# Kernel tuning notes

Hardware: AMD Instinct MI355X
Metric: run time of the kernel (lower is better)

## Reference

```python
import jax, jax.numpy as jnp
import numpy as np

EMBED_DIM = 768
NUM_HEADS = 12
HEAD_DIM = EMBED_DIM // NUM_HEADS
EPS = 1e-5  # nn.LayerNorm default


def setup_inputs() -> dict:
    key = jax.random.key(0)
    ks = jax.random.split(key, 7)
    D = EMBED_DIM
    s1 = 1.0 / np.sqrt(D)
    x = jax.random.normal(ks[0], (2, 2048, D), dtype=jnp.float32)
    # LayerNorm params
    gamma = jnp.ones((D,), jnp.float32)
    beta = jnp.zeros((D,), jnp.float32)
    # QKV projection (linear1): weight [3D, D], bias [3D]
    w1 = jax.random.uniform(ks[1], (3 * D, D), jnp.float32, -s1, s1)
    b1 = jax.random.uniform(ks[2], (3 * D,), jnp.float32, -s1, s1)
    # Output projection (linear2[0]): weight [D, D], bias [D]
    w2 = jax.random.uniform(ks[3], (D, D), jnp.float32, -s1, s1)
    b2 = jax.random.uniform(ks[4], (D,), jnp.float32, -s1, s1)
    return {"x": x, "gamma": gamma, "beta": beta, "w1": w1, "b1": b1, "w2": w2, "b2": b2}


def _layernorm(x, gamma, beta):
    mu = jnp.mean(x, axis=-1, keepdims=True)
    var = jnp.mean(jnp.square(x - mu), axis=-1, keepdims=True)
    return (x - mu) * jax.lax.rsqrt(var + EPS) * gamma + beta


def reference(x, gamma, beta, w1, b1, w2, b2) -> jnp.ndarray:
    B, L, D = x.shape
    H, Dh = NUM_HEADS, HEAD_DIM
    residual = x
    h = _layernorm(x, gamma, beta)
    qkv = h @ w1.T + b1  # [B, L, 3D]
    q, k, v = jnp.split(qkv, 3, axis=-1)
    # 'b n (h d) -> b h n d'
    q = q.reshape(B, L, H, Dh).transpose(0, 2, 1, 3)
    k = k.reshape(B, L, H, Dh).transpose(0, 2, 1, 3)
    v = v.reshape(B, L, H, Dh).transpose(0, 2, 1, 3)
    scores = jnp.einsum("bhqd,bhkd->bhqk", q, k) / jnp.sqrt(jnp.float32(Dh))
    attn = jax.nn.softmax(scores, axis=-1)  # dropout is identity in eval mode
    out = jnp.einsum("bhqk,bhkd->bhqd", attn, v)  # [B, H, L, Dh]
    out = out.transpose(0, 2, 1, 3).reshape(B, L, D)
    out = out @ w2.T + b2  # dropout identity in eval
    return residual + out
```

## Files before the change

kernel.cpp:

```cpp
#include <hip/hip_runtime.h>


#define DEV __device__ __forceinline__

typedef __attribute__((ext_vector_type(4))) float f32x4;
typedef __attribute__((ext_vector_type(8))) short s16x8;
typedef __attribute__((ext_vector_type(2))) int i32x2;

constexpr int Bb   = 2;
constexpr int Ll   = 2048;
constexpr int Dd   = 768;
constexpr int Hh   = 12;
constexpr int Dh   = 64;
constexpr int Mrows = Bb * Ll;
constexpr int N1   = 3 * Dd;

DEV unsigned short f2bf(float f) {
  union { float f; unsigned u; } v; v.f = f;
  unsigned r = v.u + 0x7fffu + ((v.u >> 16) & 1u);
  return (unsigned short)(r >> 16);
}

DEV void gload_lds16(const void* g, void* l) {
  __builtin_amdgcn_global_load_lds((const __attribute__((address_space(1))) unsigned int*)g,
                                   (__attribute__((address_space(3))) unsigned int*)l,
                                   16, 0, 0);
}

DEV f32x4 mfma16(s16x8 a, s16x8 b, f32x4 c) {
  return __builtin_amdgcn_mfma_f32_16x16x32_bf16(a, b, c, 0, 0, 0);
}

DEV float fexp2(float x) { float r; asm("v_exp_f32 %0, %1" : "=v"(r) : "v"(x)); return r; }
DEV float frcp(float x)  { float r; asm("v_rcp_f32 %0, %1" : "=v"(r) : "v"(x)); return r; }

DEV float redmax64(float x) {
  x = fmaxf(x, __shfl_xor(x, 16, 64));
  float a = x, b = x;
  asm volatile("v_permlane32_swap_b32 %0, %1" : "+v"(a), "+v"(b));
  return fmaxf(a, b);
}
DEV float redsum64(float x) {
  x += __shfl_xor(x, 16, 64);
  float a = x, b = x;
  asm volatile("v_permlane32_swap_b32 %0, %1" : "+v"(a), "+v"(b));
  return a + b;
}

DEV void ln_body(int row, int t, const float* __restrict__ x,
                 const float* __restrict__ gamma, const float* __restrict__ beta,
                 short* __restrict__ hbuf, float* red) {
  const float* xr = x + (size_t)row * Dd;
  float v0 = xr[t], v1 = xr[t + 256], v2 = xr[t + 512];
  float s = v0 + v1 + v2;
  float q = v0 * v0 + v1 * v1 + v2 * v2;
#pragma unroll
  for (int off = 32; off; off >>= 1) {
    s += __shfl_xor(s, off, 64);
    q += __shfl_xor(q, off, 64);
  }
  const int w = t >> 6, lane = t & 63;
  if (lane == 0) { red[w] = s; red[4 + w] = q; }
  __syncthreads();
  s = red[0] + red[1] + red[2] + red[3];
  q = red[4] + red[5] + red[6] + red[7];
  const float mean = s * (1.f / Dd);
  const float var  = q * (1.f / Dd) - mean * mean;
  const float rstd = rsqrtf(var + 1e-5f);
  short* hr = hbuf + (size_t)row * Dd;
  hr[t]       = (short)f2bf((v0 - mean) * rstd * gamma[t]       + beta[t]);
  hr[t + 256] = (short)f2bf((v1 - mean) * rstd * gamma[t + 256] + beta[t + 256]);
  hr[t + 512] = (short)f2bf((v2 - mean) * rstd * gamma[t + 512] + beta[t + 512]);
}

constexpr int W1E = N1 * Dd;
constexpr int W2E = Dd * Dd;

__global__ __launch_bounds__(256) void ln_kernel(const float* __restrict__ x,
                                                 const float* __restrict__ gamma,
                                                 const float* __restrict__ beta,
                                                 short* __restrict__ hbuf) {
  __shared__ float red[8];
  ln_body(blockIdx.x, threadIdx.x, x, gamma, beta, hbuf, red);
}

__global__ __launch_bounds__(256) void cvt_kernel(const float* __restrict__ w1,
                                                  const float* __restrict__ w2,
                                                  short* __restrict__ w1b,
                                                  short* __restrict__ w2b) {
  int i = blockIdx.x * 256 + threadIdx.x;
  const int stride = gridDim.x * 256;
  for (; i < W1E + W2E; i += stride) {
    if (i < W1E) w1b[i] = (short)f2bf(w1[i]);
    else         w2b[i - W1E] = (short)f2bf(w2[i - W1E]);
  }
}

__global__ __launch_bounds__(256) void prep_kernel(const float* __restrict__ x,
                                                   const float* __restrict__ gamma,
                                                   const float* __restrict__ beta,
                                                   short* __restrict__ hbuf,
                                                   const float* __restrict__ w1,
                                                   const float* __restrict__ w2,
                                                   short* __restrict__ w1b,
                                                   short* __restrict__ w2b) {
  __shared__ float red[8];
  if (blockIdx.x < (unsigned)Mrows) {
    ln_body(blockIdx.x, threadIdx.x, x, gamma, beta, hbuf, red);
  } else {
    int i = (blockIdx.x - Mrows) * 256 + threadIdx.x;
    for (; i < W1E + W2E; i += 1024 * 256) {
      if (i < W1E) w1b[i] = (short)f2bf(w1[i]);
      else         w2b[i - W1E] = (short)f2bf(w2[i - W1E]);
    }
  }
}

DEV unsigned xcd_swz(unsigned f, unsigned nwg) {
  if ((nwg & 7u) != 0u) return f;
  return (f & 7u) * (nwg >> 3) + (f >> 3);
}

template <int EPI, int WSRC>
__global__ __launch_bounds__(256) void gemm_bt(const short* __restrict__ A,
                                               const void* __restrict__ Wp,
                                               const float* __restrict__ bias,
                                               const float* __restrict__ resid,
                                               void* __restrict__ outp,
                                               int N, int K) {
  __shared__ __align__(16) short As[2][WSRC == 0 ? 128 * 32 : 128 * 64];
  __shared__ __align__(16) short Ws[2][WSRC == 0 ? 128 * 32 : 128 * 64];
  const int tid  = threadIdx.x;
  const int lane = tid & 63, wid = tid >> 6;
  const int wr = wid >> 1, wc = wid & 1;
  const int g = lane >> 4, li = lane & 15;
  const unsigned o = xcd_swz(blockIdx.y * gridDim.x + blockIdx.x,
                             gridDim.x * gridDim.y);
  const int brow = (int)(o / gridDim.x) * 128, bcol = (int)(o % gridDim.x) * 128;

  f32x4 acc[4][4];
#pragma unroll
  for (int m = 0; m < 4; ++m)
#pragma unroll
    for (int n = 0; n < 4; ++n)
#pragma unroll
      for (int r = 0; r < 4; ++r) acc[m][n][r] = 0.f;

  if constexpr (WSRC == 0) {
    const short* W = (const short*)Wp;
    const int nt = K >> 5;
    auto stage = [&](int t, int buf) {
      const int ko = t << 5;
#pragma unroll
      for (int i = 0; i < 2; ++i) {
        const int idx = i * 256 + tid;
        const int r = idx >> 2, c = idx & 3;
        const int cs = c ^ ((r >> 1) & 3);
        gload_lds16(A + (size_t)(brow + r) * K + ko + cs * 8,
                    (char*)&As[buf][0] + idx * 16);
        gload_lds16(W + (size_t)(bcol + r) * K + ko + cs * 8,
                    (char*)&Ws[buf][0] + idx * 16);
      }
    };
    stage(0, 0);
    stage(1, 1);
    for (int it = 0; it < nt; ++it) {
      const int cur = it & 1;
      if (it + 1 < nt) asm volatile("s_waitcnt vmcnt(4)" ::: "memory");
      else             asm volatile("s_waitcnt vmcnt(0)" ::: "memory");
      __builtin_amdgcn_s_barrier();
      __builtin_amdgcn_sched_barrier(0);
      {
        s16x8 af[4], bf[4];
        const int rsw = ((li >> 1) & 3);
#pragma unroll
        for (int m = 0; m < 4; ++m) {
          const int row = wr * 64 + m * 16 + li;
          af[m] = *(const s16x8*)((char*)&As[cur][0] + row * 64 + ((g ^ rsw) << 4));
        }
#pragma unroll
        for (int n = 0; n < 4; ++n) {
          const int row = wc * 64 + n * 16 + li;
          bf[n] = *(const s16x8*)((char*)&Ws[cur][0] + row * 64 + ((g ^ rsw) << 4));
        }
#pragma unroll
        for (int m = 0; m < 4; ++m)
#pragma unroll
          for (int n = 0; n < 4; ++n)
            acc[m][n] = mfma16(af[m], bf[n], acc[m][n]);
      }
      __builtin_amdgcn_s_barrier();
      if (it + 2 < nt) stage(it + 2, cur);
    }
  } else {
    const float* W = (const float*)Wp;
    for (int kt = 0; kt < K; kt += 64) {
#pragma unroll
      for (int i = 0; i < 4; ++i) {
        const int idx = i * 256 + tid;
        const int r = idx >> 3, c = idx & 7;
        const int cs = c ^ (r & 7);
        gload_lds16(A + (size_t)(brow + r) * K + kt + cs * 8,
                    (char*)&As[0][0] + idx * 16);
      }
#pragma unroll
      for (int i = 0; i < 4; ++i) {
        const int idx = i * 256 + tid;
        const int r = idx >> 3, c = idx & 7;
        const float* wp = W + (size_t)(bcol + r) * K + kt + c * 8;
        const f32x4 lo = *(const f32x4*)wp;
        const f32x4 hi = *(const f32x4*)(wp + 4);
        s16x8 oo;
#pragma unroll
        for (int j = 0; j < 4; ++j) {
          oo[j]     = (short)f2bf(lo[j]);
          oo[4 + j] = (short)f2bf(hi[j]);
        }
        *(s16x8*)((char*)&Ws[0][0] + (size_t)(r * 8 + (c ^ (r & 7))) * 16) = oo;
      }
      __syncthreads();
#pragma unroll
      for (int kk = 0; kk < 2; ++kk) {
        s16x8 af[4], bf[4];
#pragma unroll
        for (int m = 0; m < 4; ++m) {
          const int row = wr * 64 + m * 16 + li;
          af[m] = *(const s16x8*)&As[0][row * 64 + (((kk * 4 + g) ^ (li & 7)) & 7) * 8];
        }
#pragma unroll
        for (int n = 0; n < 4; ++n) {
          const int row = wc * 64 + n * 16 + li;
          bf[n] = *(const s16x8*)&Ws[0][row * 64 + (((kk * 4 + g) ^ (li & 7)) & 7) * 8];
        }
#pragma unroll
        for (int m = 0; m < 4; ++m)
#pragma unroll
          for (int n = 0; n < 4; ++n)
            acc[m][n] = mfma16(af[m], bf[n], acc[m][n]);
      }
      __syncthreads();
    }
  }

#pragma unroll
  for (int m = 0; m < 4; ++m) {
#pragma unroll
    for (int n = 0; n < 4; ++n) {
      const int col = bcol + wc * 64 + n * 16 + li;
      const float bv = bias[col];
#pragma unroll
      for (int r = 0; r < 4; ++r) {
        const int row = brow + wr * 64 + m * 16 + g * 4 + r;
        const float v = acc[m][n][r] + bv;
        if (EPI == 0) {
          ((short*)outp)[(size_t)row * N + col] = (short)f2bf(v);
        } else {
          const size_t o2 = (size_t)row * N + col;
          ((float*)outp)[o2] = v + resid[o2];
        }
      }
    }
  }
}

#define TRRD(dst, addr, OFF)                                                   \
  asm volatile("ds_read_b64_tr_b16 %0, %1 offset:" #OFF                        \
               : "=v"(dst) : "v"(addr))

__global__ __launch_bounds__(256) void attn_kernel(const short* __restrict__ qkv,
                                                   short* __restrict__ obuf) {
  __shared__ __align__(16) short Ks[2][64 * 64];
  __shared__ __align__(16) short Vt[2][64 * 64];
  __shared__ __align__(16) short Ps[4][16 * 64];
  const int tid  = threadIdx.x;
  const int lane = tid & 63, w = tid >> 6;
  const int g = lane >> 4, li = lane & 15;
  const unsigned o = xcd_swz(blockIdx.y * 32u + blockIdx.x, gridDim.x * gridDim.y);
  const int bh = (int)(o >> 5);
  const int b = bh / Hh, h = bh % Hh;
  const size_t rowbase = (size_t)b * Ll * N1;
  const int q0 = (int)(o & 31u) * 64 + w * 16;
  constexpr float kScale = 0.125f * 1.44269504f;
  constexpr float kThrRaw = 8.f / kScale;
  constexpr int KVSTRIDE = 64 * N1;

  s16x8 qf[2];
#pragma unroll
  for (int ks = 0; ks < 2; ++ks)
    qf[ks] = *(const s16x8*)(qkv + rowbase + (size_t)(q0 + li) * N1 +
                             h * Dh + ks * 32 + g * 8);

  f32x4 oa[4];
  float m_ = -1e30f, l_ = 0.f;
#pragma unroll
  for (int dn = 0; dn < 4; ++dn)
#pragma unroll
    for (int r = 0; r < 4; ++r) oa[dn][r] = 0.f;

  constexpr int NT = Ll / 64;

  const int ia = tid, ib = 256 + tid;
  const int ra = ia >> 3, ca = ia & 7, rb = ib >> 3, cb = ib & 7;
  const short* kpa = qkv + rowbase + Dd + h * Dh + (size_t)ra * N1 + (ca ^ (ra & 7)) * 8;
  const short* kpb = qkv + rowbase + Dd + h * Dh + (size_t)rb * N1 + (cb ^ (rb & 7)) * 8;
  const int Ta = ia >> 3, Tb = ib >> 3;
  const short* vpa = qkv + rowbase + 2 * Dd + h * Dh +
                     (size_t)((Ta & 15) * 4 + (ca >> 1)) * N1 + (Ta >> 4) * 16 + (ia & 1) * 8;
  const short* vpb = qkv + rowbase + 2 * Dd + h * Dh +
                     (size_t)((Tb & 15) * 4 + (cb >> 1)) * N1 + (Tb >> 4) * 16 + (ib & 1) * 8;
  char* KsB = (char*)&Ks[0][0];
  char* VtB = (char*)&Vt[0][0];
  const int dsta = ia * 16, dstb = ib * 16;

  int koff[4][2];
#pragma unroll
  for (int n = 0; n < 4; ++n) {
    koff[n][0] = ((n * 16 + li) * 64 + ((g ^ (li & 7)) & 7) * 8) * 2;
    koff[n][1] = ((n * 16 + li) * 64 + (((4 + g) ^ (li & 7)) & 7) * 8) * 2;
  }
  int pwoff[4], proff[2];
#pragma unroll
  for (int n = 0; n < 4; ++n)
    pwoff[n] = li * 128 + (((2 * n + (g >> 1)) ^ (li & 7)) << 4) + 8 * (g & 1);
#pragma unroll
  for (int kk = 0; kk < 2; ++kk)
    proff[kk] = li * 128 + (((4 * kk + g) ^ (li & 7)) << 4);
  char* Pw = (char*)&Ps[w][0];
  const unsigned vlane = (unsigned)((lane >> 4) * 256 + (lane & 15) * 2);
  const unsigned vbase0 = (unsigned)(unsigned long long)(&Vt[0][0]) + vlane;

  auto stageK = [&](int buf) {
    const int bo = buf << 13;
    gload_lds16(kpa, KsB + bo + dsta);
    gload_lds16(kpb, KsB + bo + dstb);
    kpa += KVSTRIDE; kpb += KVSTRIDE;
  };
  auto stageV = [&](int buf) {
    const int bo = buf << 13;
    gload_lds16(vpa, VtB + bo + dsta);
    gload_lds16(vpb, VtB + bo + dstb);
    vpa += KVSTRIDE; vpb += KVSTRIDE;
  };

  stageK(0); stageV(0); stageK(1); stageV(1);
  asm volatile("s_waitcnt vmcnt(4)" ::: "memory");
  __builtin_amdgcn_s_barrier();
  __builtin_amdgcn_sched_barrier(0);

  f32x4 zA[4], zB[4];
#pragma unroll
  for (int n = 0; n < 4; ++n) {
    s16x8 kf0 = *(const s16x8*)(KsB + koff[n][0]);
    s16x8 kf1 = *(const s16x8*)(KsB + koff[n][1]);
    f32x4 z;
#pragma unroll
    for (int r = 0; r < 4; ++r) z[r] = 0.f;
    z = mfma16(kf0, qf[0], z);
    z = mfma16(kf1, qf[1], z);
    zA[n] = z;
  }

  auto body = [&](int kt, int cur, f32x4 (&zC)[4], f32x4 (&zN)[4]) {
    const int curo = cur << 13;
    const int nxto = (cur ^ 1) << 13;
    if (kt + 1 < NT) asm volatile("s_waitcnt vmcnt(2)" ::: "memory");
    else             asm volatile("s_waitcnt vmcnt(0)" ::: "memory");
    __builtin_amdgcn_s_barrier();
    __builtin_amdgcn_sched_barrier(0);

    if (kt + 2 < NT) stageK(cur);

    if (kt + 1 < NT) {
      __builtin_amdgcn_s_setprio(1);
#pragma unroll
      for (int n = 0; n < 4; ++n) {
        s16x8 kf0 = *(const s16x8*)(KsB + nxto + koff[n][0]);
        s16x8 kf1 = *(const s16x8*)(KsB + nxto + koff[n][1]);
        f32x4 z;
#pragma unroll
        for (int r = 0; r < 4; ++r) z[r] = 0.f;
        z = mfma16(kf0, qf[0], z);
        z = mfma16(kf1, qf[1], z);
        zN[n] = z;
      }
      __builtin_amdgcn_s_setprio(0);
    }

    const float t0 = fmaxf(fmaxf(zC[0][0], zC[0][1]), zC[0][2]);
    const float t1 = fmaxf(fmaxf(zC[0][3], zC[1][0]), zC[1][1]);
    const float t2 = fmaxf(fmaxf(zC[1][2], zC[1][3]), zC[2][0]);
    const float t3 = fmaxf(fmaxf(zC[2][1], zC[2][2]), zC[2][3]);
    const float t4 = fmaxf(fmaxf(zC[3][0], zC[3][1]), zC[3][2]);
    const float mloc = fmaxf(fmaxf(fmaxf(fmaxf(t0, t1), t2), fmaxf(t3, t4)), zC[3][3]);
    if (!__all(mloc - m_ <= kThrRaw)) {
      const float mxr = redmax64(mloc);
      const float mnew = fmaxf(m_, mxr);
      const float sc = fexp2((m_ - mnew) * kScale);
      float scq[4];
#pragma unroll
      for (int r = 0; r < 4; ++r)
        scq[r] = __shfl(sc, (lane & 48) + ((lane & 48) >> 2) + r, 64);
#pragma unroll
      for (int dn = 0; dn < 4; ++dn)
#pragma unroll
        for (int r = 0; r < 4; ++r) oa[dn][r] *= scq[r];
      l_ *= sc;
      m_ = mnew;
    }
    const float msc = m_ * kScale;
#pragma unroll
    for (int n = 0; n < 4; ++n)
#pragma unroll
      for (int r = 0; r < 4; ++r) {
        const float p = fexp2(fmaf(zC[n][r], kScale, -msc));
        zC[n][r] = p;
        l_ += p;
      }

#pragma unroll
    for (int n = 0; n < 4; ++n) {
      unsigned u0, u1;
      asm("v_cvt_pk_bf16_f32 %0, %1, %2" : "=v"(u0) : "v"(zC[n][0]), "v"(zC[n][1]));
      asm("v_cvt_pk_bf16_f32 %0, %1, %2" : "=v"(u1) : "v"(zC[n][2]), "v"(zC[n][3]));
      i32x2 pv; pv[0] = (int)u0; pv[1] = (int)u1;
      *(i32x2*)(Pw + pwoff[n]) = pv;
    }

    s16x8 pf[2];
#pragma unroll
    for (int kk = 0; kk < 2; ++kk)
      pf[kk] = *(const s16x8*)(Pw + proff[kk]);

    union VU { long l[2]; s16x8 v; };
    VU vu[4][2];
    {
      const unsigned vaddr = vbase0 + (unsigned)curo;
      TRRD(vu[0][0].l[0], vaddr, 0);    TRRD(vu[0][0].l[1], vaddr, 128);
      TRRD(vu[0][1].l[0], vaddr, 1024); TRRD(vu[0][1].l[1], vaddr, 1152);
      TRRD(vu[1][0].l[0], vaddr, 2048); TRRD(vu[1][0].l[1], vaddr, 2176);
      TRRD(vu[1][1].l[0], vaddr, 3072); TRRD(vu[1][1].l[1], vaddr, 3200);
      TRRD(vu[2][0].l[0], vaddr, 4096); TRRD(vu[2][0].l[1], vaddr, 4224);
      TRRD(vu[2][1].l[0], vaddr, 5120); TRRD(vu[2][1].l[1], vaddr, 5248);
      TRRD(vu[3][0].l[0], vaddr, 6144); TRRD(vu[3][0].l[1], vaddr, 6272);
      TRRD(vu[3][1].l[0], vaddr, 7168); TRRD(vu[3][1].l[1], vaddr, 7296);
    }
    asm volatile("s_waitcnt lgkmcnt(0)" ::: "memory");
    __builtin_amdgcn_sched_barrier(0);

    __builtin_amdgcn_s_setprio(1);
#pragma unroll
    for (int dn = 0; dn < 4; ++dn) {
      oa[dn] = mfma16(pf[0], vu[dn][0].v, oa[dn]);
      oa[dn] = mfma16(pf[1], vu[dn][1].v, oa[dn]);
    }
    __builtin_amdgcn_s_setprio(0);

    __builtin_amdgcn_s_barrier();
    if (kt + 2 < NT) stageV(cur);
  };

  for (int g2 = 0; g2 < NT / 2; ++g2) {
    body(2 * g2,     0, zA, zB);
    body(2 * g2 + 1, 1, zB, zA);
  }

  l_ = redsum64(l_);
  {
#pragma unroll
    for (int r = 0; r < 4; ++r) {
      const float lq = __shfl(l_, (lane & 48) + ((lane & 48) >> 2) + r, 64);
      const float inv = frcp(lq);
      const int row = b * Ll + q0 + g * 4 + r;
#pragma unroll
      for (int dn = 0; dn < 4; ++dn)
        obuf[(size_t)row * Dd + h * Dh + dn * 16 + li] =
            (short)f2bf(oa[dn][r] * inv);
    }
  }
}

extern "C" void kernel_launch(void* const* d_in, const int* in_sizes, int n_in,
                              void* d_out, int out_size, void* d_ws, size_t ws_size,
                              hipStream_t stream) {
  const float* x     = (const float*)d_in[0];
  const float* gamma = (const float*)d_in[1];
  const float* beta  = (const float*)d_in[2];
  const float* w1    = (const float*)d_in[3];
  const float* b1    = (const float*)d_in[4];
  const float* w2    = (const float*)d_in[5];
  const float* b2    = (const float*)d_in[6];
  float* out = (float*)d_out;
  char* ws = (char*)d_ws;

  if (ws_size >= 29884416) {
    short* qkvb = (short*)(ws);
    short* hb   = (short*)(ws + 18874368);
    short* w1b  = (short*)(ws + 25165824);
    short* w2b  = (short*)(ws + 28704768);
    prep_kernel<<<dim3(Mrows + 1024), dim3(256), 0, stream>>>(
        x, gamma, beta, hb, w1, w2, w1b, w2b);
    gemm_bt<0, 0><<<dim3(N1 / 128, Mrows / 128), dim3(256), 0, stream>>>(
        hb, w1b, b1, nullptr, (void*)qkvb, N1, Dd);
    attn_kernel<<<dim3(Ll / 64, Bb * Hh), dim3(256), 0, stream>>>(qkvb, hb);
    gemm_bt<1, 0><<<dim3(Dd / 128, Mrows / 128), dim3(256), 0, stream>>>(
        hb, w2b, b2, x, (void*)out, Dd, Dd);
  } else if (ws_size >= 17301504) {
    short* qkvb = (short*)(ws);
    short* hb   = (short*)(ws + 9437184);
    short* w1b  = (short*)(ws + 12582912);
    short* w2b  = (short*)(ws + 16121856);
    cvt_kernel<<<dim3(1024), dim3(256), 0, stream>>>(w1, w2, w1b, w2b);
    for (int b = 0; b < Bb; ++b) {
      const size_t ro = (size_t)b * Ll * Dd;
      ln_kernel<<<dim3(Ll), dim3(256), 0, stream>>>(x + ro, gamma, beta, hb);
      gemm_bt<0, 0><<<dim3(N1 / 128, Ll / 128), dim3(256), 0, stream>>>(
          hb, w1b, b1, nullptr, (void*)qkvb, N1, Dd);
      attn_kernel<<<dim3(Ll / 64, Hh), dim3(256), 0, stream>>>(qkvb, hb);
      gemm_bt<1, 0><<<dim3(Dd / 128, Ll / 128), dim3(256), 0, stream>>>(
          hb, w2b, b2, x + ro, (void*)(out + ro), Dd, Dd);
    }
  } else {
    short* qkvb = (short*)(ws);
    short* hb   = (short*)(ws + 9437184);
    for (int b = 0; b < Bb; ++b) {
      const size_t ro = (size_t)b * Ll * Dd;
      ln_kernel<<<dim3(Ll), dim3(256), 0, stream>>>(x + ro, gamma, beta, hb);
      gemm_bt<0, 1><<<dim3(N1 / 128, Ll / 128), dim3(256), 0, stream>>>(
          hb, w1, b1, nullptr, (void*)qkvb, N1, Dd);
      attn_kernel<<<dim3(Ll / 64, Hh), dim3(256), 0, stream>>>(qkvb, hb);
      gemm_bt<1, 1><<<dim3(Dd / 128, Ll / 128), dim3(256), 0, stream>>>(
          hb, w2, b2, x + ro, (void*)(out + ro), Dd, Dd);
    }
  }
}
```

Baseline: 101.6 us.

## Split attention KV range across two wave groups and vectorize weight conversion

The attention kernel now uses 512 threads per block. Two groups of four waves each process half of the key/value sequence for the same 64 query rows, with separate double-buffered K/V tiles in shared memory. A final flash-decoding style merge combines the partial max, sum and output through LDS. Separately, the fp32-to-bf16 weight conversion now loads float4 and uses packed bf16 convert instructions instead of scalar per-element stores. The aim is more parallelism and latency hiding per query tile and a cheaper prep stage, at the cost of doubled LDS use, which may lower occupancy, plus extra merge work.

```diff
diff --git a/kernel.cpp b/kernel.cpp
--- a/kernel.cpp
+++ b/kernel.cpp
@@ -75,6 +75,20 @@
 
 constexpr int W1E = N1 * Dd;
 constexpr int W2E = Dd * Dd;
+constexpr int WV4 = (W1E + W2E) / 4;
+
+DEV void cvt_v4(int i, const float* __restrict__ w1, const float* __restrict__ w2,
+                short* __restrict__ w1b, short* __restrict__ w2b) {
+  const int e = i * 4;
+  const float* src = (e < W1E) ? (w1 + e) : (w2 + (e - W1E));
+  short* dst       = (e < W1E) ? (w1b + e) : (w2b + (e - W1E));
+  const f32x4 v = *(const f32x4*)src;
+  unsigned u01, u23;
+  asm("v_cvt_pk_bf16_f32 %0, %1, %2" : "=v"(u01) : "v"(v[0]), "v"(v[1]));
+  asm("v_cvt_pk_bf16_f32 %0, %1, %2" : "=v"(u23) : "v"(v[2]), "v"(v[3]));
+  i32x2 o; o[0] = (int)u01; o[1] = (int)u23;
+  *(i32x2*)dst = o;
+}
 
 __global__ __launch_bounds__(256) void ln_kernel(const float* __restrict__ x,
                                                  const float* __restrict__ gamma,
@@ -90,10 +104,7 @@
                                                   short* __restrict__ w2b) {
   int i = blockIdx.x * 256 + threadIdx.x;
   const int stride = gridDim.x * 256;
-  for (; i < W1E + W2E; i += stride) {
-    if (i < W1E) w1b[i] = (short)f2bf(w1[i]);
-    else         w2b[i - W1E] = (short)f2bf(w2[i - W1E]);
-  }
+  for (; i < WV4; i += stride) cvt_v4(i, w1, w2, w1b, w2b);
 }
 
 __global__ __launch_bounds__(256) void prep_kernel(const float* __restrict__ x,
@@ -109,10 +120,7 @@
     ln_body(blockIdx.x, threadIdx.x, x, gamma, beta, hbuf, red);
   } else {
     int i = (blockIdx.x - Mrows) * 256 + threadIdx.x;
-    for (; i < W1E + W2E; i += 1024 * 256) {
-      if (i < W1E) w1b[i] = (short)f2bf(w1[i]);
-      else         w2b[i - W1E] = (short)f2bf(w2[i - W1E]);
-    }
+    for (; i < WV4; i += 1024 * 256) cvt_v4(i, w1, w2, w1b, w2b);
   }
 }
 
@@ -267,22 +275,24 @@
   asm volatile("ds_read_b64_tr_b16 %0, %1 offset:" #OFF                        \
                : "=v"(dst) : "v"(addr))
 
-__global__ __launch_bounds__(256) void attn_kernel(const short* __restrict__ qkv,
+__global__ __launch_bounds__(512) void attn_kernel(const short* __restrict__ qkv,
                                                    short* __restrict__ obuf) {
-  __shared__ __align__(16) short Ks[2][64 * 64];
-  __shared__ __align__(16) short Vt[2][64 * 64];
-  __shared__ __align__(16) short Ps[4][16 * 64];
+  __shared__ __align__(16) short Ks[4][64 * 64];
+  __shared__ __align__(16) short Vt[4][64 * 64];
+  __shared__ __align__(16) short Ps[8][16 * 64];
   const int tid  = threadIdx.x;
   const int lane = tid & 63, w = tid >> 6;
+  const int wq = w & 3, kvh = w >> 2;
   const int g = lane >> 4, li = lane & 15;
   const unsigned o = xcd_swz(blockIdx.y * 32u + blockIdx.x, gridDim.x * gridDim.y);
   const int bh = (int)(o >> 5);
   const int b = bh / Hh, h = bh % Hh;
   const size_t rowbase = (size_t)b * Ll * N1;
-  const int q0 = (int)(o & 31u) * 64 + w * 16;
+  const int q0 = (int)(o & 31u) * 64 + wq * 16;
   constexpr float kScale = 0.125f * 1.44269504f;
   constexpr float kThrRaw = 8.f / kScale;
   constexpr int KVSTRIDE = 64 * N1;
+  constexpr int NT2 = 16;
 
   s16x8 qf[2];
 #pragma unroll
@@ -297,19 +307,19 @@
 #pragma unroll
     for (int r = 0; r < 4; ++r) oa[dn][r] = 0.f;
 
-  constexpr int NT = Ll / 64;
-
-  const int ia = tid, ib = 256 + tid;
+  const int lt = tid & 255;
+  const int ia = lt, ib = 256 + lt;
   const int ra = ia >> 3, ca = ia & 7, rb = ib >> 3, cb = ib & 7;
-  const short* kpa = qkv + rowbase + Dd + h * Dh + (size_t)ra * N1 + (ca ^ (ra & 7)) * 8;
-  const short* kpb = qkv + rowbase + Dd + h * Dh + (size_t)rb * N1 + (cb ^ (rb & 7)) * 8;
+  const size_t hb0 = rowbase + (size_t)(kvh * NT2) * KVSTRIDE;
+  const short* kpa = qkv + hb0 + Dd + h * Dh + (size_t)ra * N1 + (ca ^ (ra & 7)) * 8;
+  const short* kpb = qkv + hb0 + Dd + h * Dh + (size_t)rb * N1 + (cb ^ (rb & 7)) * 8;
   const int Ta = ia >> 3, Tb = ib >> 3;
-  const short* vpa = qkv + rowbase + 2 * Dd + h * Dh +
+  const short* vpa = qkv + hb0 + 2 * Dd + h * Dh +
                      (size_t)((Ta & 15) * 4 + (ca >> 1)) * N1 + (Ta >> 4) * 16 + (ia & 1) * 8;
-  const short* vpb = qkv + rowbase + 2 * Dd + h * Dh +
+  const short* vpb = qkv + hb0 + 2 * Dd + h * Dh +
                      (size_t)((Tb & 15) * 4 + (cb >> 1)) * N1 + (Tb >> 4) * 16 + (ib & 1) * 8;
-  char* KsB = (char*)&Ks[0][0];
-  char* VtB = (char*)&Vt[0][0];
+  char* KsB = (char*)&Ks[0][0] + (kvh << 14);
+  char* VtB = (char*)&Vt[0][0] + (kvh << 14);
   const int dsta = ia * 16, dstb = ib * 16;
 
   int koff[4][2];
@@ -327,7 +337,7 @@
     proff[kk] = li * 128 + (((4 * kk + g) ^ (li & 7)) << 4);
   char* Pw = (char*)&Ps[w][0];
   const unsigned vlane = (unsigned)((lane >> 4) * 256 + (lane & 15) * 2);
-  const unsigned vbase0 = (unsigned)(unsigned long long)(&Vt[0][0]) + vlane;
+  const unsigned vbase0 = (unsigned)(unsigned long long)VtB + vlane;
 
   auto stageK = [&](int buf) {
     const int bo = buf << 13;
@@ -363,14 +373,14 @@
   auto body = [&](int kt, int cur, f32x4 (&zC)[4], f32x4 (&zN)[4]) {
     const int curo = cur << 13;
     const int nxto = (cur ^ 1) << 13;
-    if (kt + 1 < NT) asm volatile("s_waitcnt vmcnt(2)" ::: "memory");
-    else             asm volatile("s_waitcnt vmcnt(0)" ::: "memory");
+    if (kt + 1 < NT2) asm volatile("s_waitcnt vmcnt(2)" ::: "memory");
+    else              asm volatile("s_waitcnt vmcnt(0)" ::: "memory");
     __builtin_amdgcn_s_barrier();
     __builtin_amdgcn_sched_barrier(0);
 
-    if (kt + 2 < NT) stageK(cur);
-
-    if (kt + 1 < NT) {
+    if (kt + 2 < NT2) stageK(cur);
+
+    if (kt + 1 < NT2) {
       __builtin_amdgcn_s_setprio(1);
 #pragma unroll
       for (int n = 0; n < 4; ++n) {
@@ -456,25 +466,49 @@
     __builtin_amdgcn_s_setprio(0);
 
     __builtin_amdgcn_s_barrier();
-    if (kt + 2 < NT) stageV(cur);
+    if (kt + 2 < NT2) stageV(cur);
   };
 
-  for (int g2 = 0; g2 < NT / 2; ++g2) {
+  for (int g2 = 0; g2 < NT2 / 2; ++g2) {
     body(2 * g2,     0, zA, zB);
     body(2 * g2 + 1, 1, zB, zA);
   }
 
   l_ = redsum64(l_);
-  {
+  __syncthreads();
+  float* MO = (float*)&Ks[0][0];
+  float* MM = (float*)&Vt[0][0];
+  if (kvh == 1) {
+#pragma unroll
+    for (int dn = 0; dn < 4; ++dn)
+#pragma unroll
+      for (int r = 0; r < 4; ++r)
+        MO[wq * 1024 + (g * 4 + r) * 64 + dn * 16 + li] = oa[dn][r];
+    if (g == 0) {
+      MM[wq * 16 + li] = m_;
+      MM[64 + wq * 16 + li] = l_;
+    }
+  }
+  __syncthreads();
+  if (kvh == 0) {
 #pragma unroll
     for (int r = 0; r < 4; ++r) {
-      const float lq = __shfl(l_, (lane & 48) + ((lane & 48) >> 2) + r, 64);
-      const float inv = frcp(lq);
-      const int row = b * Ll + q0 + g * 4 + r;
-#pragma unroll
-      for (int dn = 0; dn < 4; ++dn)
+      const int qr = g * 4 + r;
+      const float m0 = __shfl(m_, (lane & 48) + qr, 64);
+      const float l0 = __shfl(l_, (lane & 48) + qr, 64);
+      const float m1 = MM[wq * 16 + qr];
+      const float l1 = MM[64 + wq * 16 + qr];
+      const float mm = fmaxf(m0, m1);
+      const float s0 = fexp2((m0 - mm) * kScale);
+      const float s1 = fexp2((m1 - mm) * kScale);
+      const float inv = frcp(l0 * s0 + l1 * s1);
+      const int row = b * Ll + q0 + qr;
+#pragma unroll
+      for (int dn = 0; dn < 4; ++dn) {
+        const float o1 = MO[wq * 1024 + qr * 64 + dn * 16 + li];
         obuf[(size_t)row * Dd + h * Dh + dn * 16 + li] =
-            (short)f2bf(oa[dn][r] * inv);
+            (short)f2bf((oa[dn][r] * s0 + o1 * s1) * inv);
+      }
     }
   }
 }
@@ -501,7 +535,7 @@
         x, gamma, beta, hb, w1, w2, w1b, w2b);
     gemm_bt<0, 0><<<dim3(N1 / 128, Mrows / 128), dim3(256), 0, stream>>>(
         hb, w1b, b1, nullptr, (void*)qkvb, N1, Dd);
-    attn_kernel<<<dim3(Ll / 64, Bb * Hh), dim3(256), 0, stream>>>(qkvb, hb);
+    attn_kernel<<<dim3(Ll / 64, Bb * Hh), dim3(512), 0, stream>>>(qkvb, hb);
     gemm_bt<1, 0><<<dim3(Dd / 128, Mrows / 128), dim3(256), 0, stream>>>(
         hb, w2b, b2, x, (void*)out, Dd, Dd);
   } else if (ws_size >= 17301504) {
@@ -515,7 +549,7 @@
       ln_kernel<<<dim3(Ll), dim3(256), 0, stream>>>(x + ro, gamma, beta, hb);
       gemm_bt<0, 0><<<dim3(N1 / 128, Ll / 128), dim3(256), 0, stream>>>(
           hb, w1b, b1, nullptr, (void*)qkvb, N1, Dd);
-      attn_kernel<<<dim3(Ll / 64, Hh), dim3(256), 0, stream>>>(qkvb, hb);
+      attn_kernel<<<dim3(Ll / 64, Hh), dim3(512), 0, stream>>>(qkvb, hb);
       gemm_bt<1, 0><<<dim3(Dd / 128, Ll / 128), dim3(256), 0, stream>>>(
           hb, w2b, b2, x + ro, (void*)(out + ro), Dd, Dd);
     }
@@ -527,7 +561,7 @@
       ln_kernel<<<dim3(Ll), dim3(256), 0, stream>>>(x + ro, gamma, beta, hb);
       gemm_bt<0, 1><<<dim3(N1 / 128, Ll / 128), dim3(256), 0, stream>>>(
           hb, w1, b1, nullptr, (void*)qkvb, N1, Dd);
-      attn_kernel<<<dim3(Ll / 64, Hh), dim3(256), 0, stream>>>(qkvb, hb);
+      attn_kernel<<<dim3(Ll / 64, Hh), dim3(512), 0, stream>>>(qkvb, hb);
       gemm_bt<1, 1><<<dim3(Dd / 128, Ll / 128), dim3(256), 0, stream>>>(
           hb, w2, b2, x + ro, (void*)(out + ro), Dd, Dd);
     }
```

Result: slower. 116.7 us (+14.9%).
